# Kernel optimization log

Hardware: AMD Instinct MI355X
Metric: run time of the kernel (lower is better)

Reference implementation:

```python
import jax, jax.numpy as jnp
import numpy as np

B_, S, D_IN, D_OUT = 4, 2048, 4096, 4096
N, RANK, ALPHA = 8, 16, 32
SCALE = ALPHA / RANK


def setup_inputs() -> dict:
    key = jax.random.key(0)
    kx, ka, kb, kw, kbias = jax.random.split(key, 5)
    x = jax.random.normal(kx, (B_, S, D_IN), dtype=jnp.float32)
    # lora_A.weight: [rank, in_features]; lora_B.weight: [out_features, rank]
    lora_A = jax.random.normal(ka, (N, RANK, D_IN), dtype=jnp.float32) * (1.0 / np.sqrt(D_IN))
    lora_B = jax.random.normal(kb, (N, D_OUT, RANK), dtype=jnp.float32) * (1.0 / np.sqrt(RANK))
    W = jax.random.normal(kw, (D_OUT, D_IN), dtype=jnp.float32) * (1.0 / np.sqrt(D_IN))
    bias = jax.random.normal(kbias, (D_OUT,), dtype=jnp.float32) * 0.01
    lora_weights = jnp.full((N,), 1.0 / N, dtype=jnp.float32)  # param_weight init
    return {"x": x, "lora_A": lora_A, "lora_B": lora_B, "W": W,
            "bias": bias, "lora_weights": lora_weights}


def reference(x, lora_A, lora_B, W, bias, lora_weights):
    # Dropout(p=0.01) treated as identity (eval mode) for deterministic reference.
    # low-rank projections for all adapters at once: [n, b, s, r]
    h = jnp.einsum('bsd,nrd->nbsr', x, lora_A)
    # up-projection with per-adapter scale * learned weight fused into B
    coef = (SCALE * lora_weights)[:, None, None]           # [n,1,1]
    lora_out = jnp.einsum('nbsr,nor->bso', h, lora_B * coef)
    base = jnp.einsum('bsd,od->bso', x, W) + bias
    return base + lora_out
```

## Files before the change

### kernel.cpp

```cpp
#include <hip/hip_runtime.h>
#include <hip/hip_bf16.h>
#include <stdint.h>


typedef __attribute__((ext_vector_type(4))) float f32x4;
typedef __attribute__((ext_vector_type(8))) __bf16 bf16x8;
typedef __attribute__((ext_vector_type(8))) unsigned short u16x8;

#define GLOBAL_AS(p) ((const __attribute__((address_space(1))) void*)(p))
#define LDS_AS(p)    ((__attribute__((address_space(3))) void*)(p))

__device__ __forceinline__ ushort f2b(float f) {
    __hip_bfloat16 h = __float2bfloat16(f);
    ushort u;
    __builtin_memcpy(&u, &h, 2);
    return u;
}

__global__ void prep_kernel(const float* __restrict__ lA,
                            const float* __restrict__ lB,
                            const float* __restrict__ lw,
                            ushort* __restrict__ Bcat,
                            ushort* __restrict__ AcatT)
{
    int idx = blockIdx.x * 256 + threadIdx.x;
    int o = idx >> 7, k = idx & 127;
    int n = k >> 4, r = k & 15;
    Bcat[idx]  = f2b(2.0f * lw[n] * lB[((size_t)n * 4096 + o) * 16 + r]);
    AcatT[idx] = f2b(lA[(size_t)k * 4096 + o]);
}

__global__ void cvtx_kernel(const float* __restrict__ x, ushort* __restrict__ xb) {
    size_t i = ((size_t)blockIdx.x * 256 + threadIdx.x) * 8;
    const float4* xf = (const float4*)(x + i);
    float4 a = xf[0], b = xf[1];
    u16x8 r;
    r[0] = f2b(a.x); r[1] = f2b(a.y); r[2] = f2b(a.z); r[3] = f2b(a.w);
    r[4] = f2b(b.x); r[5] = f2b(b.y); r[6] = f2b(b.z); r[7] = f2b(b.w);
    *reinterpret_cast<u16x8*>(xb + i) = r;
}

template <bool OUT_F32, bool ADD_BIAS, bool ADD_C>
__global__ __launch_bounds__(256) void gemm_bt(
    const ushort* __restrict__ Amat, const ushort* __restrict__ Bmat,
    const float* __restrict__ aux, void* __restrict__ OutP,
    int M, int N, int K)
{
    constexpr int BM = 128, BN = 128, BK = 32;
    __shared__ __align__(16) ushort As[BM * BK];
    __shared__ __align__(16) ushort Bs[BN * BK];

    const int tid  = threadIdx.x;
    const int lane = tid & 63;
    const int w    = tid >> 6;
    const int wm   = (w >> 1) * 64;
    const int wn   = (w & 1) * 64;
    const int quad = lane >> 4;
    const int lrow = lane & 15;
    const int m0 = blockIdx.x * BM;
    const int n0 = blockIdx.y * BN;

    const int srow = (w * 2) * 16 + (lane >> 2);
    const int kofs = (lane & 3) * 8;
    const ushort* agp0 = Amat + (size_t)(m0 + srow) * K + kofs;
    const ushort* agp1 = agp0 + (size_t)16 * K;
    const ushort* bgp0 = Bmat + (size_t)(n0 + srow) * K + kofs;
    const ushort* bgp1 = bgp0 + (size_t)16 * K;
    ushort* lA0 = &As[(w * 2) * 512];
    ushort* lA1 = &As[(w * 2 + 1) * 512];
    ushort* lB0 = &Bs[(w * 2) * 512];
    ushort* lB1 = &Bs[(w * 2 + 1) * 512];

    f32x4 acc[4][4] = {};
    const int nK = K / BK;
    for (int kt = 0; kt < nK; ++kt) {
        __syncthreads();
        __builtin_amdgcn_global_load_lds(GLOBAL_AS(agp0), LDS_AS(lA0), 16, 0, 0);
        __builtin_amdgcn_global_load_lds(GLOBAL_AS(agp1), LDS_AS(lA1), 16, 0, 0);
        __builtin_amdgcn_global_load_lds(GLOBAL_AS(bgp0), LDS_AS(lB0), 16, 0, 0);
        __builtin_amdgcn_global_load_lds(GLOBAL_AS(bgp1), LDS_AS(lB1), 16, 0, 0);
        agp0 += BK; agp1 += BK; bgp0 += BK; bgp1 += BK;
        __syncthreads();

        bf16x8 af[4], bfr[4];
#pragma unroll
        for (int i = 0; i < 4; ++i)
            af[i] = *reinterpret_cast<const bf16x8*>(&As[(wm + i * 16 + lrow) * BK + quad * 8]);
#pragma unroll
        for (int j = 0; j < 4; ++j)
            bfr[j] = *reinterpret_cast<const bf16x8*>(&Bs[(wn + j * 16 + lrow) * BK + quad * 8]);
#pragma unroll
        for (int i = 0; i < 4; ++i)
#pragma unroll
            for (int j = 0; j < 4; ++j)
                acc[i][j] = __builtin_amdgcn_mfma_f32_16x16x32_bf16(af[i], bfr[j], acc[i][j], 0, 0, 0);
    }

#pragma unroll
    for (int i = 0; i < 4; ++i) {
        const int row = m0 + wm + i * 16 + quad * 4;
#pragma unroll
        for (int j = 0; j < 4; ++j) {
            const int col = n0 + wn + j * 16 + lrow;
            float badd = ADD_BIAS ? aux[col] : 0.0f;
#pragma unroll
            for (int v = 0; v < 4; ++v) {
                float val = acc[i][j][v] + badd;
                if (ADD_C) val += aux[(size_t)(row + v) * N + col];
                if (OUT_F32)
                    ((float*)OutP)[(size_t)(row + v) * N + col] = val;
                else
                    ((ushort*)OutP)[(size_t)(row + v) * N + col] = f2b(val);
            }
        }
    }
}

__global__ __launch_bounds__(256) void gemm_af32(
    const float* __restrict__ Af, const ushort* __restrict__ Bmat,
    const float* __restrict__ bias, float* __restrict__ Out,
    int M, int N, int K)
{
    constexpr int BM = 128, BN = 128, BK = 32;
    __shared__ __align__(16) ushort As[BM * BK];
    __shared__ __align__(16) ushort Bs[BN * BK];

    const int tid  = threadIdx.x;
    const int lane = tid & 63;
    const int w    = tid >> 6;
    const int wm   = (w >> 1) * 64;
    const int wn   = (w & 1) * 64;
    const int quad = lane >> 4;
    const int lrow = lane & 15;
    const int m0 = blockIdx.x * BM;
    const int n0 = blockIdx.y * BN;

    const int srow = (w * 2) * 16 + (lane >> 2);
    const int kofs = (lane & 3) * 8;
    const ushort* bgp0 = Bmat + (size_t)(n0 + srow) * K + kofs;
    const ushort* bgp1 = bgp0 + (size_t)16 * K;
    ushort* lB0 = &Bs[(w * 2) * 512];
    ushort* lB1 = &Bs[(w * 2 + 1) * 512];

    f32x4 acc[4][4] = {};
    const int nK = K / BK;
    for (int kt = 0; kt < nK; ++kt) {
        __syncthreads();
        __builtin_amdgcn_global_load_lds(GLOBAL_AS(bgp0), LDS_AS(lB0), 16, 0, 0);
        __builtin_amdgcn_global_load_lds(GLOBAL_AS(bgp1), LDS_AS(lB1), 16, 0, 0);
        bgp0 += BK; bgp1 += BK;
#pragma unroll
        for (int gg = 0; gg < 2; ++gg) {
            int g = tid + gg * 256;
            int row = g >> 2, kc = (g & 3) * 8;
            const float* src = Af + (size_t)(m0 + row) * K + (size_t)kt * BK + kc;
            float4 a = *(const float4*)src;
            float4 b = *(const float4*)(src + 4);
            u16x8 r;
            r[0] = f2b(a.x); r[1] = f2b(a.y); r[2] = f2b(a.z); r[3] = f2b(a.w);
            r[4] = f2b(b.x); r[5] = f2b(b.y); r[6] = f2b(b.z); r[7] = f2b(b.w);
            *reinterpret_cast<u16x8*>(&As[row * BK + kc]) = r;
        }
        __syncthreads();

        bf16x8 af[4], bfr[4];
#pragma unroll
        for (int i = 0; i < 4; ++i)
            af[i] = *reinterpret_cast<const bf16x8*>(&As[(wm + i * 16 + lrow) * BK + quad * 8]);
#pragma unroll
        for (int j = 0; j < 4; ++j)
            bfr[j] = *reinterpret_cast<const bf16x8*>(&Bs[(wn + j * 16 + lrow) * BK + quad * 8]);
#pragma unroll
        for (int i = 0; i < 4; ++i)
#pragma unroll
            for (int j = 0; j < 4; ++j)
                acc[i][j] = __builtin_amdgcn_mfma_f32_16x16x32_bf16(af[i], bfr[j], acc[i][j], 0, 0, 0);
    }

#pragma unroll
    for (int i = 0; i < 4; ++i) {
        const int row = m0 + wm + i * 16 + quad * 4;
#pragma unroll
        for (int j = 0; j < 4; ++j) {
            const int col = n0 + wn + j * 16 + lrow;
            float badd = bias[col];
#pragma unroll
            for (int v = 0; v < 4; ++v)
                Out[(size_t)(row + v) * N + col] = acc[i][j][v] + badd;
        }
    }
}

__global__ void naive_kernel(const float* __restrict__ x, const float* __restrict__ lA,
                             const float* __restrict__ lB, const float* __restrict__ W,
                             const float* __restrict__ bias, const float* __restrict__ lw,
                             float* __restrict__ out)
{
    __shared__ float xs[4096];
    __shared__ float h[128];
    const int m = blockIdx.x;
    for (int d = threadIdx.x; d < 4096; d += 256)
        xs[d] = x[(size_t)m * 4096 + d];
    __syncthreads();
    for (int k = threadIdx.x; k < 128; k += 256) {
        const float* arow = lA + (size_t)k * 4096;
        float s = 0.f;
        for (int d = 0; d < 4096; ++d) s += xs[d] * arow[d];
        h[k] = s;
    }
    __syncthreads();
    for (int o = threadIdx.x; o < 4096; o += 256) {
        const float* wrow = W + (size_t)o * 4096;
        float s = bias[o];
        for (int d = 0; d < 4096; ++d) s += xs[d] * wrow[d];
        for (int n = 0; n < 8; ++n) {
            const float* brow = lB + ((size_t)n * 4096 + o) * 16;
            float t = 0.f;
            for (int r = 0; r < 16; ++r) t += h[n * 16 + r] * brow[r];
            s += 2.0f * lw[n] * t;
        }
        out[(size_t)m * 4096 + o] = s;
    }
}

extern "C" void kernel_launch(void* const* d_in, const int* in_sizes, int n_in,
                              void* d_out, int out_size, void* d_ws, size_t ws_size,
                              hipStream_t stream)
{
    const float* x    = (const float*)d_in[0];
    const float* lA   = (const float*)d_in[1];
    const float* lB   = (const float*)d_in[2];
    const float* W    = (const float*)d_in[3];
    const float* bias = (const float*)d_in[4];
    const float* lw   = (const float*)d_in[5];
    float* out = (float*)d_out;

    ushort* Bcat  = (ushort*)d_ws;
    ushort* AcatT = Bcat + (size_t)4096 * 128;
    ushort* Weff  = AcatT + (size_t)4096 * 128;
    ushort* xb    = Weff + (size_t)4096 * 4096;
    const size_t need_t2 = (2 * (size_t)4096 * 128 + (size_t)4096 * 4096) * 2;
    const size_t need_t1 = need_t2 + (size_t)8192 * 4096 * 2;

    if (ws_size >= need_t2) {
        prep_kernel<<<2048, 256, 0, stream>>>(lA, lB, lw, Bcat, AcatT);
        gemm_bt<false, false, true><<<dim3(32, 32), 256, 0, stream>>>(
            Bcat, AcatT, W, Weff, 4096, 4096, 128);
        if (ws_size >= need_t1) {
            cvtx_kernel<<<16384, 256, 0, stream>>>(x, xb);
            gemm_bt<true, true, false><<<dim3(64, 32), 256, 0, stream>>>(
                xb, Weff, bias, out, 8192, 4096, 4096);
        } else {
            gemm_af32<<<dim3(64, 32), 256, 0, stream>>>(
                x, Weff, bias, out, 8192, 4096, 4096);
        }
    } else {
        naive_kernel<<<8192, 256, 0, stream>>>(x, lA, lB, W, bias, lw, out);
    }
}
```

Measured before the change: 655.3 us.

## Double the GEMM K-step per barrier and transpose lora_A via LDS tile

The main bf16 GEMM now loads two 32-wide K slices into LDS per iteration and runs both MFMA halves between one pair of barriers. This halves the barrier and loop overhead per unit of K at the cost of twice the LDS footprint. The prep kernel is split so the lora_A transpose goes through a shared-memory tile, giving coalesced reads and vectorized writes in place of strided global reads. Since K must now be a multiple of 64, a K that is not would silently drop work, but 4096 and 128 both qualify.

Result: no change. 650.4 us (-0.7%).

```diff
diff --git a/kernel.cpp b/kernel.cpp
--- a/kernel.cpp
+++ b/kernel.cpp
@@ -17,17 +17,37 @@
     return u;
 }
 
-__global__ void prep_kernel(const float* __restrict__ lA,
-                            const float* __restrict__ lB,
-                            const float* __restrict__ lw,
-                            ushort* __restrict__ Bcat,
-                            ushort* __restrict__ AcatT)
+__global__ __launch_bounds__(256) void prep_a_kernel(const float* __restrict__ lA,
+                                                     ushort* __restrict__ AcatT) {
+    __shared__ ushort tile[64][136];
+    const int tid = threadIdx.x;
+    const int d0 = blockIdx.x * 64;
+#pragma unroll
+    for (int it = 0; it < 32; ++it) {
+        int k = it * 4 + (tid >> 6);
+        int dc = tid & 63;
+        tile[dc][k] = f2b(lA[(size_t)k * 4096 + d0 + dc]);
+    }
+    __syncthreads();
+#pragma unroll
+    for (int it = 0; it < 4; ++it) {
+        int g = it * 256 + tid;
+        int dc = g >> 4, slot = g & 15;
+        u16x8 v;
+#pragma unroll
+        for (int e = 0; e < 8; ++e) v[e] = tile[dc][slot * 8 + e];
+        *reinterpret_cast<u16x8*>(&AcatT[((size_t)(d0 + dc)) * 128 + slot * 8]) = v;
+    }
+}
+
+__global__ void prep_b_kernel(const float* __restrict__ lB,
+                              const float* __restrict__ lw,
+                              ushort* __restrict__ Bcat)
 {
     int idx = blockIdx.x * 256 + threadIdx.x;
     int o = idx >> 7, k = idx & 127;
     int n = k >> 4, r = k & 15;
-    Bcat[idx]  = f2b(2.0f * lw[n] * lB[((size_t)n * 4096 + o) * 16 + r]);
-    AcatT[idx] = f2b(lA[(size_t)k * 4096 + o]);
+    Bcat[idx] = f2b(2.0f * lw[n] * lB[((size_t)n * 4096 + o) * 16 + r]);
 }
 
 __global__ void cvtx_kernel(const float* __restrict__ x, ushort* __restrict__ xb) {
@@ -46,9 +66,9 @@
     const float* __restrict__ aux, void* __restrict__ OutP,
     int M, int N, int K)
 {
-    constexpr int BM = 128, BN = 128, BK = 32;
-    __shared__ __align__(16) ushort As[BM * BK];
-    __shared__ __align__(16) ushort Bs[BN * BK];
+    constexpr int BK = 32;
+    __shared__ __align__(16) ushort As[2 * 128 * BK];
+    __shared__ __align__(16) ushort Bs[2 * 128 * BK];
 
     const int tid  = threadIdx.x;
     const int lane = tid & 63;
@@ -57,8 +77,8 @@
     const int wn   = (w & 1) * 64;
     const int quad = lane >> 4;
     const int lrow = lane & 15;
-    const int m0 = blockIdx.x * BM;
-    const int n0 = blockIdx.y * BN;
+    const int m0 = blockIdx.x * 128;
+    const int n0 = blockIdx.y * 128;
 
     const int srow = (w * 2) * 16 + (lane >> 2);
     const int kofs = (lane & 3) * 8;
@@ -66,34 +86,43 @@
     const ushort* agp1 = agp0 + (size_t)16 * K;
     const ushort* bgp0 = Bmat + (size_t)(n0 + srow) * K + kofs;
     const ushort* bgp1 = bgp0 + (size_t)16 * K;
-    ushort* lA0 = &As[(w * 2) * 512];
-    ushort* lA1 = &As[(w * 2 + 1) * 512];
-    ushort* lB0 = &Bs[(w * 2) * 512];
-    ushort* lB1 = &Bs[(w * 2 + 1) * 512];
+    ushort* lA00 = &As[(w * 2) * 512];
+    ushort* lA01 = &As[(w * 2 + 1) * 512];
+    ushort* lB00 = &Bs[(w * 2) * 512];
+    ushort* lB01 = &Bs[(w * 2 + 1) * 512];
 
     f32x4 acc[4][4] = {};
-    const int nK = K / BK;
+    const int nK = K >> 6;
     for (int kt = 0; kt < nK; ++kt) {
         __syncthreads();
-        __builtin_amdgcn_global_load_lds(GLOBAL_AS(agp0), LDS_AS(lA0), 16, 0, 0);
-        __builtin_amdgcn_global_load_lds(GLOBAL_AS(agp1), LDS_AS(lA1), 16, 0, 0);
-        __builtin_amdgcn_global_load_lds(GLOBAL_AS(bgp0), LDS_AS(lB0), 16, 0, 0);
-        __builtin_amdgcn_global_load_lds(GLOBAL_AS(bgp1), LDS_AS(lB1), 16, 0, 0);
-        agp0 += BK; agp1 += BK; bgp0 += BK; bgp1 += BK;
-        __syncthreads();
-
-        bf16x8 af[4], bfr[4];
-#pragma unroll
-        for (int i = 0; i < 4; ++i)
-            af[i] = *reinterpret_cast<const bf16x8*>(&As[(wm + i * 16 + lrow) * BK + quad * 8]);
-#pragma unroll
-        for (int j = 0; j < 4; ++j)
-            bfr[j] = *reinterpret_cast<const bf16x8*>(&Bs[(wn + j * 16 + lrow) * BK + quad * 8]);
-#pragma unroll
-        for (int i = 0; i < 4; ++i)
+        __builtin_amdgcn_global_load_lds(GLOBAL_AS(agp0),      LDS_AS(lA00),        16, 0, 0);
+        __builtin_amdgcn_global_load_lds(GLOBAL_AS(agp1),      LDS_AS(lA01),        16, 0, 0);
+        __builtin_amdgcn_global_load_lds(GLOBAL_AS(agp0 + 32), LDS_AS(lA00 + 4096), 16, 0, 0);
+        __builtin_amdgcn_global_load_lds(GLOBAL_AS(agp1 + 32), LDS_AS(lA01 + 4096), 16, 0, 0);
+        __builtin_amdgcn_global_load_lds(GLOBAL_AS(bgp0),      LDS_AS(lB00),        16, 0, 0);
+        __builtin_amdgcn_global_load_lds(GLOBAL_AS(bgp1),      LDS_AS(lB01),        16, 0, 0);
+        __builtin_amdgcn_global_load_lds(GLOBAL_AS(bgp0 + 32), LDS_AS(lB00 + 4096), 16, 0, 0);
+        __builtin_amdgcn_global_load_lds(GLOBAL_AS(bgp1 + 32), LDS_AS(lB01 + 4096), 16, 0, 0);
+        agp0 += 64; agp1 += 64; bgp0 += 64; bgp1 += 64;
+        __syncthreads();
+
+#pragma unroll
+        for (int h = 0; h < 2; ++h) {
+            const ushort* ab = &As[h * 4096];
+            const ushort* bb = &Bs[h * 4096];
+            bf16x8 af[4], bfr[4];
+#pragma unroll
+            for (int i = 0; i < 4; ++i)
+                af[i] = *reinterpret_cast<const bf16x8*>(&ab[(wm + i * 16 + lrow) * BK + quad * 8]);
 #pragma unroll
             for (int j = 0; j < 4; ++j)
-                acc[i][j] = __builtin_amdgcn_mfma_f32_16x16x32_bf16(af[i], bfr[j], acc[i][j], 0, 0, 0);
+                bfr[j] = *reinterpret_cast<const bf16x8*>(&bb[(wn + j * 16 + lrow) * BK + quad * 8]);
+#pragma unroll
+            for (int i = 0; i < 4; ++i)
+#pragma unroll
+                for (int j = 0; j < 4; ++j)
+                    acc[i][j] = __builtin_amdgcn_mfma_f32_16x16x32_bf16(af[i], bfr[j], acc[i][j], 0, 0, 0);
+        }
     }
 
 #pragma unroll
@@ -243,7 +272,8 @@
     const size_t need_t1 = need_t2 + (size_t)8192 * 4096 * 2;
 
     if (ws_size >= need_t2) {
-        prep_kernel<<<2048, 256, 0, stream>>>(lA, lB, lw, Bcat, AcatT);
+        prep_a_kernel<<<64, 256, 0, stream>>>(lA, AcatT);
+        prep_b_kernel<<<2048, 256, 0, stream>>>(lB, lw, Bcat);
         gemm_bt<false, false, true><<<dim3(32, 32), 256, 0, stream>>>(
             Bcat, AcatT, W, Weff, 4096, 4096, 128);
         if (ws_size >= need_t1) {
```
